# Kernel tuning notes

Hardware: AMD Instinct MI355X
Metric: run time of the kernel (lower is better)

The kernel has to match this reference:

```python
import jax, jax.numpy as jnp
import numpy as np

D_MODEL = 1024
H = 16
D_K = D_MODEL // H
D_FF = 4096
EPS = 1e-6
NEG = -1.0e9


def setup_inputs() -> dict:
    key = jax.random.key(0)
    ks = jax.random.split(key, 8)
    B, S = 4, 2048
    x = jax.random.normal(ks[0], (B, S, D_MODEL), dtype=jnp.float32)
    src_mask = jnp.ones((B, 1, S, S), dtype=jnp.int32)
    s = 0.02
    wq = jax.random.normal(ks[1], (D_MODEL, D_MODEL), jnp.float32) * s
    wk = jax.random.normal(ks[2], (D_MODEL, D_MODEL), jnp.float32) * s
    wv = jax.random.normal(ks[3], (D_MODEL, D_MODEL), jnp.float32) * s
    wo = jax.random.normal(ks[4], (D_MODEL, D_MODEL), jnp.float32) * s
    w1 = jax.random.normal(ks[5], (D_MODEL, D_FF), jnp.float32) * s
    b1 = jnp.zeros((D_FF,), jnp.float32)
    w2 = jax.random.normal(ks[6], (D_FF, D_MODEL), jnp.float32) * s
    b2 = jnp.zeros((D_MODEL,), jnp.float32)
    # LayerNorm params are scalars in the original (torch.ones(1)/zeros(1))
    a1 = jnp.ones((1,), jnp.float32); bt1 = jnp.zeros((1,), jnp.float32)
    a2 = jnp.ones((1,), jnp.float32); bt2 = jnp.zeros((1,), jnp.float32)
    return {"x": x, "src_mask": src_mask, "wq": wq, "wk": wk, "wv": wv,
            "wo": wo, "w1": w1, "b1": b1, "w2": w2, "b2": b2,
            "a1": a1, "bt1": bt1, "a2": a2, "bt2": bt2}


def _layernorm(x, alpha, beta):
    # Original: (x - mean) / (std + eps), std with Bessel correction (torch default)
    mean = jnp.mean(x, axis=-1, keepdims=True)
    std = jnp.std(x, axis=-1, keepdims=True, ddof=1)
    return alpha * (x - mean) / (std + EPS) + beta


def _mha(x, mask, wq, wk, wv, wo):
    B, S, _ = x.shape
    q = (x @ wq).reshape(B, S, H, D_K).transpose(0, 2, 1, 3)  # [B,H,S,Dk]
    k = (x @ wk).reshape(B, S, H, D_K).transpose(0, 2, 1, 3)
    v = (x @ wv).reshape(B, S, H, D_K).transpose(0, 2, 1, 3)
    scores = jnp.einsum('bhqd,bhkd->bhqk', q, k) / jnp.sqrt(jnp.float32(D_K))
    scores = jnp.where(mask == 0, NEG, scores)
    attn = jax.nn.softmax(scores, axis=-1)
    out = jnp.einsum('bhqk,bhkd->bhqd', attn, v)  # [B,H,S,Dk]
    out = out.transpose(0, 2, 1, 3).reshape(B, S, D_MODEL)
    return out @ wo


def reference(x, src_mask, wq, wk, wv, wo, w1, b1, w2, b2, a1, bt1, a2, bt2):
    # Sublayer 1: self-attention with post-norm residual (dropout = eval/identity)
    attn_out = _mha(x, src_mask, wq, wk, wv, wo)
    x = _layernorm(x + attn_out, a1, bt1)
    # Sublayer 2: FFN with post-norm residual
    ffn_out = jax.nn.relu(x @ w1 + b1) @ w2 + b2
    x = _layernorm(x + ffn_out, a2, bt2)
    return x
```

## Files before the change

kernel.cpp:

```cpp
#include <hip/hip_runtime.h>
#include <stdint.h>

typedef __bf16 bf16x8 __attribute__((ext_vector_type(8)));
typedef float f32x4 __attribute__((ext_vector_type(4)));
typedef float f32x16 __attribute__((ext_vector_type(16)));
typedef unsigned short u16;
typedef u16 u16x8 __attribute__((ext_vector_type(8)));
typedef u16 u16x4 __attribute__((ext_vector_type(4)));
typedef uint32_t u32;

#define DEV __device__ __forceinline__
#define MFMA(a, b, c) __builtin_amdgcn_mfma_f32_16x16x32_bf16(a, b, c, 0, 0, 0)
#define MFMA32(a, b, c) __builtin_amdgcn_mfma_f32_32x32x16_bf16(a, b, c, 0, 0, 0)

static constexpr int B_ = 4, S_ = 2048, M_ = 8192, D_ = 1024, H_ = 16, DFF_ = 4096;

DEV u16 f2bf(float f) {
    union { float f; u32 u; } c; c.f = f;
    u32 u = c.u;
    return (u16)((u + 0x7fffu + ((u >> 16) & 1u)) >> 16);
}

DEV u32 cvt_pk_bf16(float lo, float hi) {
    u32 r;
    asm("v_cvt_pk_bf16_f32 %0, %1, %2" : "=v"(r) : "v"(lo), "v"(hi));
    return r;
}

DEV float v_exp2(float x) {
    float r;
    asm("v_exp_f32 %0, %1" : "=v"(r) : "v"(x));
    return r;
}

DEV void gload16(void* lds, const void* g) {
    __builtin_amdgcn_global_load_lds(
        (const __attribute__((address_space(1))) unsigned int*)g,
        (__attribute__((address_space(3))) unsigned int*)lds, 16, 0, 0);
}


__global__ __launch_bounds__(256) void k_pack_mask(const int* __restrict__ m,
                                                   u32* __restrict__ bits, int nwords) {
    int w = blockIdx.x * 256 + threadIdx.x;
    if (w >= nwords) return;
    const int4* s = (const int4*)(m + (size_t)w * 32);
    u32 r = 0;
#pragma unroll
    for (int j = 0; j < 8; j++) {
        int4 v = s[j];
        r |= (u32)(v.x != 0) << (j * 4) | (u32)(v.y != 0) << (j * 4 + 1) |
             (u32)(v.z != 0) << (j * 4 + 2) | (u32)(v.w != 0) << (j * 4 + 3);
    }
    bits[w] = r;
}

__global__ __launch_bounds__(256) void k_cast_bf16(const float* __restrict__ s,
                                                   u16* __restrict__ d, int n4) {
    int i = blockIdx.x * 256 + threadIdx.x;
    if (i >= n4) return;
    f32x4 v = ((const f32x4*)s)[i];
    u16x4 o;
    o[0] = f2bf(v[0]); o[1] = f2bf(v[1]); o[2] = f2bf(v[2]); o[3] = f2bf(v[3]);
    ((u16x4*)d)[i] = o;
}

__global__ void k_transpose_cast(const float* __restrict__ s, u16* __restrict__ d,
                                 int K, int N) {
    __shared__ float t[32][33];
    int n0 = blockIdx.x * 32, k0 = blockIdx.y * 32;
    int tx = threadIdx.x, ty = threadIdx.y;
#pragma unroll
    for (int i = 0; i < 4; i++)
        t[ty + i * 8][tx] = s[(size_t)(k0 + ty + i * 8) * N + n0 + tx];
    __syncthreads();
#pragma unroll
    for (int i = 0; i < 4; i++)
        d[(size_t)(n0 + ty + i * 8) * K + k0 + tx] = f2bf(t[tx][ty + i * 8]);
}

__global__ void k_transpose_cast4(const float* __restrict__ s0,
                                  const float* __restrict__ s1,
                                  const float* __restrict__ s2,
                                  const float* __restrict__ s3,
                                  u16* __restrict__ dbase) {
    __shared__ float t[32][33];
    const int z = blockIdx.z;
    const float* s = (z == 0) ? s0 : (z == 1) ? s1 : (z == 2) ? s2 : s3;
    u16* d = dbase + (size_t)z * D_ * D_;
    int n0 = blockIdx.x * 32, k0 = blockIdx.y * 32;
    int tx = threadIdx.x, ty = threadIdx.y;
#pragma unroll
    for (int i = 0; i < 4; i++)
        t[ty + i * 8][tx] = s[(size_t)(k0 + ty + i * 8) * D_ + n0 + tx];
    __syncthreads();
#pragma unroll
    for (int i = 0; i < 4; i++)
        d[(size_t)(n0 + ty + i * 8) * D_ + k0 + tx] = f2bf(t[tx][ty + i * 8]);
}

template <int EPI>
__global__ __launch_bounds__(512, 4) void k_gemm8(const u16* __restrict__ A,
                                                  const u16* __restrict__ Bt,
                                                  float* __restrict__ Cf,
                                                  u16* __restrict__ Cb,
                                                  const float* __restrict__ bias,
                                                  const float* __restrict__ resid,
                                                  u16* __restrict__ Vt,
                                                  int N, int K) {
    __shared__ u16 As[2][128 * 64];
    __shared__ u16 Bs[2][128 * 64];
    const int tid = threadIdx.x, lane = tid & 63, wave = tid >> 6;
    const int lr = lane & 15, lg = lane >> 4;
    const int wm = wave >> 1, wn = wave & 1;
    const int nbx = N >> 7;
    const int chunk = gridDim.x >> 3;
    const int id = ((int)blockIdx.x & 7) * chunk + ((int)blockIdx.x >> 3);
    const size_t row0 = (size_t)(id / nbx) * 128;
    const int col0 = (id % nbx) * 128;
    const int srow = lane >> 3;
    const int sgr = (lane & 7) ^ srow;
    const int NT = K >> 6;
    f32x4 acc[2][4] = {};

    auto stage = [&](int buf, int t) {
#pragma unroll
        for (int i = 0; i < 2; i++) {
            int c = i * 8 + wave;
            gload16((char*)&As[buf][0] + c * 1024,
                    (const char*)(A + (row0 + c * 8 + srow) * K + t * 64 + sgr * 8));
        }
#pragma unroll
        for (int i = 0; i < 2; i++) {
            int c = i * 8 + wave;
            gload16((char*)&Bs[buf][0] + c * 1024,
                    (const char*)(Bt + (size_t)(col0 + c * 8 + srow) * K + t * 64 + sgr * 8));
        }
    };

    stage(0, 0);
    for (int t = 0; t < NT; ++t) {
        const int cur = t & 1;
        if (t + 1 < NT) {
            stage(cur ^ 1, t + 1);
            asm volatile("s_waitcnt vmcnt(4)" ::: "memory");
        } else {
            asm volatile("s_waitcnt vmcnt(0)" ::: "memory");
        }
        __builtin_amdgcn_s_barrier();
        asm volatile("" ::: "memory");
        bf16x8 bF[4][2];
#pragma unroll
        for (int n = 0; n < 4; n++) {
            int r = wn * 64 + n * 16 + lr;
            int rb = r * 128, sw = (r & 7) << 4;
#pragma unroll
            for (int ks = 0; ks < 2; ks++)
                bF[n][ks] = *(const bf16x8*)((char*)&Bs[cur][0] +
                                             (rb + ((ks * 64 + lg * 16) ^ sw)));
        }
#pragma unroll
        for (int m = 0; m < 2; m++) {
            int r = wm * 32 + m * 16 + lr;
            int rb = r * 128, sw = (r & 7) << 4;
            bf16x8 a0 = *(const bf16x8*)((char*)&As[cur][0] + (rb + ((lg * 16) ^ sw)));
            bf16x8 a1 = *(const bf16x8*)((char*)&As[cur][0] + (rb + ((64 + lg * 16) ^ sw)));
            __builtin_amdgcn_s_setprio(1);
#pragma unroll
            for (int n = 0; n < 4; n++) {
                acc[m][n] = MFMA(a0, bF[n][0], acc[m][n]);
                acc[m][n] = MFMA(a1, bF[n][1], acc[m][n]);
            }
            __builtin_amdgcn_s_setprio(0);
        }
        asm volatile("" ::: "memory");
        __builtin_amdgcn_s_barrier();
    }
#pragma unroll
    for (int m = 0; m < 2; m++)
#pragma unroll
        for (int n = 0; n < 4; n++) {
            const int cg = col0 + wn * 64 + n * 16 + lr;
            const int rbase = (int)row0 + wm * 32 + m * 16 + lg * 4;
            if constexpr (EPI == 0) {
                const int proj = cg >> 10, hh = (cg >> 6) & 15, dk = cg & 63;
                const int b = rbase >> 11, s = rbase & 2047;
                if (proj == 2) {
                    u16x4 ov;
#pragma unroll
                    for (int i = 0; i < 4; i++) ov[i] = f2bf(acc[m][n][i]);
                    *(u16x4*)(Vt + ((size_t)(b * 16 + hh) * 64 + dk) * 2048 + s) = ov;
                } else {
                    const float sc = (proj == 0) ? 0.1803368801111832f : 1.f;
                    size_t base = ((size_t)(proj * 64 + b * 16 + hh) * 2048 + s) * 64 + dk;
#pragma unroll
                    for (int i = 0; i < 4; i++)
                        Cb[base + (size_t)i * 64] = f2bf(acc[m][n][i] * sc);
                }
            } else {
#pragma unroll
                for (int i = 0; i < 4; i++) {
                    const int rg = rbase + i;
                    float v = acc[m][n][i];
                    if constexpr (EPI == 1) {
                        Cf[(size_t)rg * N + cg] = v + resid[(size_t)rg * N + cg];
                    } else if constexpr (EPI == 2) {
                        v += bias[cg];
                        v = v > 0.f ? v : 0.f;
                        Cb[(size_t)rg * N + cg] = f2bf(v);
                    } else {
                        Cf[(size_t)rg * N + cg] = v + bias[cg] + resid[(size_t)rg * N + cg];
                    }
                }
            }
        }
}

template <int EPI, int KSPLITS>
__global__ __launch_bounds__(512, 2) void k_gemm256(const u16* __restrict__ A,
                                                    const u16* __restrict__ Bt,
                                                    float* __restrict__ Cf,
                                                    float* __restrict__ Cf2,
                                                    u16* __restrict__ Cb,
                                                    const float* __restrict__ bias,
                                                    int N, int Keff, int lda) {
    __shared__ u16 As[2][256 * 64];
    __shared__ u16 Bs[2][256 * 64];
    const int tid = threadIdx.x, lane = tid & 63, wave = tid >> 6;
    const int lr = lane & 15, lg = lane >> 4;
    const int wm = wave >> 2, wn = wave & 3;
    const int nbx = N >> 8;
    const int chunk = gridDim.x >> 3;
    const int id = ((int)blockIdx.x & 7) * chunk + ((int)blockIdx.x >> 3);
    int tileid = id, ksplit = 0;
    if constexpr (KSPLITS == 2) { ksplit = id & 1; tileid = id >> 1; }
    const int kof = ksplit * Keff;
    const size_t row0 = (size_t)(tileid / nbx) * 256;
    const int col0 = (tileid % nbx) * 256;
    const int srow = lane >> 3;
    const int sgr = (lane & 7) ^ srow;
    const int NT = Keff >> 6;
    f32x4 acc[8][4] = {};

    auto stage_half = [&](int isB, int buf, int t, int h) {
        const u16* g = isB ? Bt : A;
        const size_t grow0 = isB ? (size_t)col0 : row0;
        char* base = isB ? (char*)&Bs[buf][0] : (char*)&As[buf][0];
#pragma unroll
        for (int l = 0; l < 2; l++) {
            int rt = h * 128 + l * 64 + wave * 8;
            gload16(base + rt * 128,
                    (const char*)(g + (grow0 + rt + srow) * lda + kof + t * 64 + sgr * 8));
        }
    };
    auto rdA = [&](int cur, int mh, int m, int kk) -> bf16x8 {
        int r = wm * 128 + mh * 64 + m * 16 + lr;
        int gi = kk * 4 + lg;
        return *(const bf16x8*)((char*)&As[cur][0] + r * 128 + ((gi ^ (r & 7)) << 4));
    };
    auto rdB = [&](int cur, int nh, int n, int kk) -> bf16x8 {
        int r = wn * 64 + nh * 32 + n * 16 + lr;
        int gi = kk * 4 + lg;
        return *(const bf16x8*)((char*)&Bs[cur][0] + r * 128 + ((gi ^ (r & 7)) << 4));
    };

    stage_half(0, 0, 0, 0); stage_half(0, 0, 0, 1);
    stage_half(1, 0, 0, 0); stage_half(1, 0, 0, 1);
    stage_half(1, 1, 1, 0); stage_half(1, 1, 1, 1);
    asm volatile("s_waitcnt vmcnt(4)" ::: "memory");
    __builtin_amdgcn_s_barrier();

    bf16x8 aF[4][2], b0F[2][2], b1F[2][2];
    for (int t = 0; t < NT; ++t) {
        const int cur = t & 1, nxt = cur ^ 1;
#pragma unroll
        for (int m = 0; m < 4; m++) { aF[m][0] = rdA(cur, 0, m, 0); aF[m][1] = rdA(cur, 0, m, 1); }
#pragma unroll
        for (int n = 0; n < 2; n++) { b0F[n][0] = rdB(cur, 0, n, 0); b0F[n][1] = rdB(cur, 0, n, 1); }
        if (t + 1 < NT) stage_half(0, nxt, t + 1, 0);
        __builtin_amdgcn_s_barrier();
        asm volatile("s_waitcnt lgkmcnt(0)" ::: "memory");
        __builtin_amdgcn_sched_barrier(0);
        __builtin_amdgcn_s_setprio(1);
#pragma unroll
        for (int m = 0; m < 4; m++)
#pragma unroll
            for (int n = 0; n < 2; n++) {
                acc[m][n] = MFMA(aF[m][0], b0F[n][0], acc[m][n]);
                acc[m][n] = MFMA(aF[m][1], b0F[n][1], acc[m][n]);
            }
        __builtin_amdgcn_s_setprio(0);
        __builtin_amdgcn_s_barrier();
#pragma unroll
        for (int n = 0; n < 2; n++) { b1F[n][0] = rdB(cur, 1, n, 0); b1F[n][1] = rdB(cur, 1, n, 1); }
        if (t + 1 < NT) stage_half(0, nxt, t + 1, 1);
        __builtin_amdgcn_s_barrier();
        asm volatile("s_waitcnt lgkmcnt(0)" ::: "memory");
        __builtin_amdgcn_sched_barrier(0);
        __builtin_amdgcn_s_setprio(1);
#pragma unroll
        for (int m = 0; m < 4; m++)
#pragma unroll
            for (int n = 0; n < 2; n++) {
                acc[m][2 + n] = MFMA(aF[m][0], b1F[n][0], acc[m][2 + n]);
                acc[m][2 + n] = MFMA(aF[m][1], b1F[n][1], acc[m][2 + n]);
            }
        __builtin_amdgcn_s_setprio(0);
        __builtin_amdgcn_s_barrier();
#pragma unroll
        for (int m = 0; m < 4; m++) { aF[m][0] = rdA(cur, 1, m, 0); aF[m][1] = rdA(cur, 1, m, 1); }
        if (t + 2 < NT) stage_half(1, cur, t + 2, 0);
        __builtin_amdgcn_s_barrier();
        asm volatile("s_waitcnt lgkmcnt(0)" ::: "memory");
        __builtin_amdgcn_sched_barrier(0);
        __builtin_amdgcn_s_setprio(1);
#pragma unroll
        for (int m = 0; m < 4; m++)
#pragma unroll
            for (int n = 0; n < 2; n++) {
                acc[4 + m][2 + n] = MFMA(aF[m][0], b1F[n][0], acc[4 + m][2 + n]);
                acc[4 + m][2 + n] = MFMA(aF[m][1], b1F[n][1], acc[4 + m][2 + n]);
            }
        __builtin_amdgcn_s_setprio(0);
        __builtin_amdgcn_s_barrier();
        if (t + 2 < NT) stage_half(1, cur, t + 2, 1);
        if (t + 1 < NT) {
            if (t + 2 < NT) asm volatile("s_waitcnt vmcnt(4)" ::: "memory");
            else            asm volatile("s_waitcnt vmcnt(0)" ::: "memory");
        }
        __builtin_amdgcn_s_barrier();
        __builtin_amdgcn_s_setprio(1);
#pragma unroll
        for (int m = 0; m < 4; m++)
#pragma unroll
            for (int n = 0; n < 2; n++) {
                acc[4 + m][n] = MFMA(aF[m][0], b0F[n][0], acc[4 + m][n]);
                acc[4 + m][n] = MFMA(aF[m][1], b0F[n][1], acc[4 + m][n]);
            }
        __builtin_amdgcn_s_setprio(0);
        __builtin_amdgcn_s_barrier();
    }
    float* Cout = (KSPLITS == 2 && ksplit) ? Cf2 : Cf;
#pragma unroll
    for (int m = 0; m < 8; m++)
#pragma unroll
        for (int n = 0; n < 4; n++)
#pragma unroll
            for (int i = 0; i < 4; i++) {
                int rg = (int)row0 + wm * 128 + m * 16 + lg * 4 + i;
                int cg = col0 + wn * 64 + n * 16 + lr;
                float v = acc[m][n][i];
                if constexpr (EPI == 2) {
                    v += bias[cg];
                    v = v > 0.f ? v : 0.f;
                    Cb[(size_t)rg * N + cg] = f2bf(v);
                } else {
                    Cout[(size_t)rg * N + cg] = v;
                }
            }
}

__global__ __launch_bounds__(256) void k_attn(const u16* __restrict__ qkv,
                                              const u16* __restrict__ vT,
                                              const u32* __restrict__ mbits,
                                              u16* __restrict__ outb) {
    __shared__ u16 Kt[2][64 * 64];
    __shared__ u16 Vt[2][64 * 64];
    __shared__ u32 pm[2][128][2];
    const int tid = threadIdx.x, lane = tid & 63, wave = tid >> 6;
    const int l31 = lane & 31, hi = lane >> 5;
    const int id0 = blockIdx.y * 16 + blockIdx.x;
    const int id = (id0 & 7) * 128 + (id0 >> 3);
    const int bh = id >> 4;
    const int b = bh >> 4, h = bh & 15;
    const int qb0 = (id & 15) * 128;
    const size_t qbase = (size_t)bh * (2048 * 64);
    const size_t kbase = (size_t)(64 + bh) * (2048 * 64);
    const size_t vtbase = (size_t)bh * (64 * 2048);

    bf16x8 qf[4];
    const int q0 = qb0 + wave * 32;
#pragma unroll
    for (int dstep = 0; dstep < 4; dstep++)
        qf[dstep] = *(const bf16x8*)(qkv + qbase + (size_t)(q0 + l31) * 64 +
                                     dstep * 16 + hi * 8);

    u16x8 ones_u;
#pragma unroll
    for (int e = 0; e < 8; e++) ones_u[e] = 0x3f80;
    const bf16x8 ones8 = *(const bf16x8*)&ones_u;

    f32x16 o0 = {}, o1 = {}, lacc = {};
    f32x16 zin;
#pragma unroll
    for (int r = 0; r < 16; r++) zin[r] = -16.f;

    const int str = tid >> 2, sq = tid & 3;
    const int swzs = (str & 7) << 4;

    u16x8 krA, krB, vrA, vrB; u32 mwA;
    auto issue_loads = [&](int kv0n) {
        const u16* ksrc = qkv + kbase + (size_t)(kv0n + str) * 64 + sq * 16;
        krA = *(const u16x8*)ksrc; krB = *(const u16x8*)(ksrc + 8);
        const u16* vsrc = vT + vtbase + (size_t)str * 2048 + kv0n + sq * 16;
        vrA = *(const u16x8*)vsrc; vrB = *(const u16x8*)(vsrc + 8);
        mwA = mbits[(size_t)(b * 2048 + qb0 + (tid >> 1)) * 64 + (kv0n >> 5) + (tid & 1)];
    };
    auto write_tile = [&](int buf) -> bool {
        int b0 = str * 128 + sq * 32;
        *(u16x8*)((char*)&Kt[buf][0] + ((b0) ^ swzs)) = krA;
        *(u16x8*)((char*)&Kt[buf][0] + ((b0 + 16) ^ swzs)) = krB;
        *(u16x8*)((char*)&Vt[buf][0] + ((b0) ^ swzs)) = vrA;
        *(u16x8*)((char*)&Vt[buf][0] + ((b0 + 16) ^ swzs)) = vrB;
        pm[buf][tid >> 1][tid & 1] = mwA;
        return (__ballot(mwA == 0xffffffffu) == ~0ull);
    };

    const int rK0 = l31, rK1 = 32 + l31;
    const int swK0 = (rK0 & 7) << 4, swK1 = (rK1 & 7) << 4;

    issue_loads(0);
    bool aon_nxt = write_tile(0);
    for (int t = 0; t < 32; ++t) {
        const int cur = t & 1;
        const bool aon_cur = aon_nxt;
        if (t + 1 < 32) issue_loads((t + 1) * 64);
        asm volatile("s_waitcnt lgkmcnt(0)" ::: "memory");
        __builtin_amdgcn_s_barrier();

        f32x16 st0 = zin, st1 = zin;
        __builtin_amdgcn_s_setprio(1);
#pragma unroll
        for (int dstep = 0; dstep < 4; dstep++) {
            bf16x8 kf0 = *(const bf16x8*)((char*)&Kt[cur][0] + rK0 * 128 +
                                          ((dstep * 32 + hi * 16) ^ swK0));
            bf16x8 kf1 = *(const bf16x8*)((char*)&Kt[cur][0] + rK1 * 128 +
                                          ((dstep * 32 + hi * 16) ^ swK1));
            st0 = MFMA32(kf0, qf[dstep], st0);
            st1 = MFMA32(kf1, qf[dstep], st1);
        }
        __builtin_amdgcn_s_setprio(0);

        if (!aon_cur) {
            u32 mw0 = pm[cur][wave * 32 + l31][0] >> (hi * 4);
            u32 mw1 = pm[cur][wave * 32 + l31][1] >> (hi * 4);
#pragma unroll
            for (int r = 0; r < 16; r++) {
                int sh = (r & 3) + 8 * (r >> 2);
                if (!((mw0 >> sh) & 1u)) st0[r] = -1e9f;
                if (!((mw1 >> sh) & 1u)) st1[r] = -1e9f;
            }
        }
        bf16x8 pa[4];
#pragma unroll
        for (int r = 0; r < 16; r++) { st0[r] = v_exp2(st0[r]); st1[r] = v_exp2(st1[r]); }
#pragma unroll
        for (int kvb = 0; kvb < 2; kvb++) {
            const f32x16& st = kvb ? st1 : st0;
            u32 wA[4], wB[4];
#pragma unroll
            for (int g = 0; g < 4; g++) {
                wA[g] = cvt_pk_bf16(st[4 * g], st[4 * g + 1]);
                wB[g] = cvt_pk_bf16(st[4 * g + 2], st[4 * g + 3]);
            }
#pragma unroll
            for (int s = 0; s < 2; s++) {
                u32 xA = wA[2 * s], yA = wA[2 * s + 1];
                asm("v_permlane32_swap_b32 %0, %1" : "+v"(xA), "+v"(yA));
                u32 xB = wB[2 * s], yB = wB[2 * s + 1];
                asm("v_permlane32_swap_b32 %0, %1" : "+v"(xB), "+v"(yB));
                union { u32 w[4]; bf16x8 v; } pk;
                pk.w[0] = xA; pk.w[1] = xB; pk.w[2] = yA; pk.w[3] = yB;
                pa[kvb * 2 + s] = pk.v;
            }
        }
        __builtin_amdgcn_s_setprio(1);
#pragma unroll
        for (int ks = 0; ks < 4; ks++) {
            bf16x8 vb0 = *(const bf16x8*)((char*)&Vt[cur][0] + rK0 * 128 +
                                          ((ks * 32 + hi * 16) ^ swK0));
            bf16x8 vb1 = *(const bf16x8*)((char*)&Vt[cur][0] + rK1 * 128 +
                                          ((ks * 32 + hi * 16) ^ swK1));
            lacc = MFMA32(pa[ks], ones8, lacc);
            o0 = MFMA32(pa[ks], vb0, o0);
            o1 = MFMA32(pa[ks], vb1, o1);
        }
        __builtin_amdgcn_s_setprio(0);
        if (t + 1 < 32) aon_nxt = write_tile(cur ^ 1);
    }
#pragma unroll
    for (int r = 0; r < 16; r++) {
        float inv = 1.f / lacc[r];
        int qg = qb0 + wave * 32 + (r & 3) + 8 * (r >> 2) + 4 * hi;
        size_t rowb = (size_t)(b * 2048 + qg) * 1024 + h * 64 + l31;
        outb[rowb] = f2bf(o0[r] * inv);
        outb[rowb + 32] = f2bf(o1[r] * inv);
    }
}

template <bool WB>
__global__ __launch_bounds__(256) void k_ln(const float* __restrict__ tin,
                                            float* __restrict__ outf,
                                            u16* __restrict__ outb,
                                            const float* __restrict__ alpha,
                                            const float* __restrict__ beta) {
    const int row = blockIdx.x, tid = threadIdx.x;
    const f32x4 t = ((const f32x4*)(tin + (size_t)row * 1024))[tid];
    float s = t[0] + t[1] + t[2] + t[3];
    float ss = t[0] * t[0] + t[1] * t[1] + t[2] * t[2] + t[3] * t[3];
#pragma unroll
    for (int m2 = 1; m2 < 64; m2 <<= 1) {
        s += __shfl_xor(s, m2);
        ss += __shfl_xor(ss, m2);
    }
    __shared__ float ps[4], pss[4];
    if ((tid & 63) == 0) { ps[tid >> 6] = s; pss[tid >> 6] = ss; }
    __syncthreads();
    s = ps[0] + ps[1] + ps[2] + ps[3];
    ss = pss[0] + pss[1] + pss[2] + pss[3];
    const float mean = s * (1.f / 1024.f);
    float var = (ss - 1024.f * mean * mean) * (1.f / 1023.f);
    var = fmaxf(var, 0.f);
    const float inv = alpha[0] / (sqrtf(var) + 1e-6f);
    const float bet = beta[0];
    f32x4 oo;
#pragma unroll
    for (int i = 0; i < 4; i++) oo[i] = (t[i] - mean) * inv + bet;
    ((f32x4*)(outf + (size_t)row * 1024))[tid] = oo;
    if constexpr (WB) {
        u16x4 ob;
#pragma unroll
        for (int i = 0; i < 4; i++) ob[i] = f2bf(oo[i]);
        ((u16x4*)(outb + (size_t)row * 1024))[tid] = ob;
    }
}

__global__ __launch_bounds__(256) void k_ln_sum2(const float* __restrict__ p0,
                                                 const float* __restrict__ p1,
                                                 const float* __restrict__ resid,
                                                 const float* __restrict__ bias,
                                                 float* __restrict__ outf,
                                                 const float* __restrict__ alpha,
                                                 const float* __restrict__ beta) {
    const int row = blockIdx.x, tid = threadIdx.x;
    const f32x4 a = ((const f32x4*)(p0 + (size_t)row * 1024))[tid];
    const f32x4 c = ((const f32x4*)(p1 + (size_t)row * 1024))[tid];
    const f32x4 r = ((const f32x4*)(resid + (size_t)row * 1024))[tid];
    const f32x4 bb = ((const f32x4*)bias)[tid];
    f32x4 t;
#pragma unroll
    for (int i = 0; i < 4; i++) t[i] = a[i] + c[i] + r[i] + bb[i];
    float s = t[0] + t[1] + t[2] + t[3];
    float ss = t[0] * t[0] + t[1] * t[1] + t[2] * t[2] + t[3] * t[3];
#pragma unroll
    for (int m2 = 1; m2 < 64; m2 <<= 1) {
        s += __shfl_xor(s, m2);
        ss += __shfl_xor(ss, m2);
    }
    __shared__ float ps[4], pss[4];
    if ((tid & 63) == 0) { ps[tid >> 6] = s; pss[tid >> 6] = ss; }
    __syncthreads();
    s = ps[0] + ps[1] + ps[2] + ps[3];
    ss = pss[0] + pss[1] + pss[2] + pss[3];
    const float mean = s * (1.f / 1024.f);
    float var = (ss - 1024.f * mean * mean) * (1.f / 1023.f);
    var = fmaxf(var, 0.f);
    const float inv = alpha[0] / (sqrtf(var) + 1e-6f);
    const float bet = beta[0];
    f32x4 oo;
#pragma unroll
    for (int i = 0; i < 4; i++) oo[i] = (t[i] - mean) * inv + bet;
    ((f32x4*)(outf + (size_t)row * 1024))[tid] = oo;
}

extern "C" void kernel_launch(void* const* d_in, const int* in_sizes, int n_in,
                              void* d_out, int out_size, void* d_ws, size_t ws_size,
                              hipStream_t stream) {
    const float* x   = (const float*)d_in[0];
    const int*   msk = (const int*)d_in[1];
    const float* wq  = (const float*)d_in[2];
    const float* wk  = (const float*)d_in[3];
    const float* wv  = (const float*)d_in[4];
    const float* wo  = (const float*)d_in[5];
    const float* w1  = (const float*)d_in[6];
    const float* b1  = (const float*)d_in[7];
    const float* w2  = (const float*)d_in[8];
    const float* b2  = (const float*)d_in[9];
    const float* a1  = (const float*)d_in[10];
    const float* bt1 = (const float*)d_in[11];
    const float* a2  = (const float*)d_in[12];
    const float* bt2 = (const float*)d_in[13];
    float* out = (float*)d_out;

    char* ws = (char*)d_ws;
    size_t off = 0;
    auto alloc = [&](size_t bytes) {
        void* p = ws + off;
        off += (bytes + 255) & ~(size_t)255;
        return p;
    };
    u16* xb    = (u16*)alloc((size_t)M_ * D_ * 2);
    u16* wqkvT = (u16*)alloc((size_t)3 * D_ * D_ * 2);
    u16* woT   = (u16*)alloc((size_t)D_ * D_ * 2);
    u16* w1T   = (u16*)alloc((size_t)DFF_ * D_ * 2);
    u16* w2T   = (u16*)alloc((size_t)D_ * DFF_ * 2);
    u32* mbits = (u32*)alloc((size_t)B_ * S_ * 64 * 4);
    u16* aout  = (u16*)alloc((size_t)M_ * D_ * 2);
    float* y   = (float*)alloc((size_t)M_ * D_ * 4);
    float* y1  = (float*)alloc((size_t)M_ * D_ * 4);
    float* x1  = (float*)alloc((size_t)M_ * D_ * 4);
    u16* x1b   = (u16*)alloc((size_t)M_ * D_ * 2);
    u16* vTb   = (u16*)alloc((size_t)64 * 64 * 2048 * 2);
    u16* qkv   = (u16*)alloc((size_t)M_ * DFF_ * 2);
    u16* hft   = qkv;

    k_pack_mask<<<dim3((B_ * S_ * 64) / 256), 256, 0, stream>>>(msk, mbits, B_ * S_ * 64);
    k_cast_bf16<<<dim3((M_ * D_ / 4) / 256), 256, 0, stream>>>(x, xb, M_ * D_ / 4);
    dim3 tb(32, 8);
    k_transpose_cast4<<<dim3(32, 32, 4), tb, 0, stream>>>(wq, wk, wv, wo, wqkvT);
    k_transpose_cast<<<dim3(128, 32), tb, 0, stream>>>(w1, w1T, D_, DFF_);
    k_transpose_cast<<<dim3(32, 128), tb, 0, stream>>>(w2, w2T, DFF_, D_);

    k_gemm8<0><<<dim3(1536), 512, 0, stream>>>(xb, wqkvT, nullptr, qkv, nullptr,
                                               nullptr, vTb, 3 * D_, D_);
    k_attn<<<dim3(16, 64), 256, 0, stream>>>(qkv, vTb, mbits, aout);
    k_gemm8<1><<<dim3(512), 512, 0, stream>>>(aout, woT, y, nullptr, nullptr, x,
                                              nullptr, D_, D_);
    k_ln<true><<<dim3(M_), 256, 0, stream>>>(y, x1, x1b, a1, bt1);
    k_gemm256<2, 1><<<dim3(512), 512, 0, stream>>>(x1b, w1T, nullptr, nullptr, hft,
                                                   b1, DFF_, D_, D_);
    k_gemm256<3, 2><<<dim3(256), 512, 0, stream>>>(hft, w2T, y, y1, nullptr,
                                                   nullptr, D_, DFF_ / 2, DFF_);
    k_ln_sum2<<<dim3(M_), 256, 0, stream>>>(y, y1, x1, b2, out, a2, bt2);
}
```

Baseline: 412.2 us.

## Stage attention K/V via direct-to-LDS loads and carry residuals in bf16

The attention kernel now loads K and V tiles with global_load_lds straight into swizzled LDS, replacing the register round-trip. It also uses a precomputed per-row all-ones mask bitmap (new k_amask kernel) so mask words are read only for tiles that are not fully unmasked. The Wo GEMM epilogue writes its residual sum as bf16, the first LayerNorm reads bf16 and emits only a bf16 output, and the final LayerNorm takes its residual from that bf16 buffer, which cuts fp32 traffic. Trade-offs: an extra barrier per iteration, one more small kernel, and lower precision in the residual path.

```diff
diff --git a/kernel.cpp b/kernel.cpp
--- a/kernel.cpp
+++ b/kernel.cpp
@@ -21,6 +21,11 @@
     return (u16)((u + 0x7fffu + ((u >> 16) & 1u)) >> 16);
 }
 
+DEV float bf2f(u16 v) {
+    union { u32 u; float f; } c; c.u = (u32)v << 16;
+    return c.f;
+}
+
 DEV u32 cvt_pk_bf16(float lo, float hi) {
     u32 r;
     asm("v_cvt_pk_bf16_f32 %0, %1, %2" : "=v"(r) : "v"(lo), "v"(hi));
@@ -53,6 +58,21 @@
              (u32)(v.z != 0) << (j * 4 + 2) | (u32)(v.w != 0) << (j * 4 + 3);
     }
     bits[w] = r;
+}
+
+__global__ __launch_bounds__(256) void k_amask(const u32* __restrict__ bits,
+                                               u32* __restrict__ am, int rows) {
+    int row = blockIdx.x * 256 + threadIdx.x;
+    if (row >= rows) return;
+    const uint4* p = (const uint4*)(bits + (size_t)row * 64);
+    u32 r = 0;
+#pragma unroll
+    for (int j = 0; j < 16; j++) {
+        uint4 v = p[j];
+        r |= (u32)((v.x & v.y) == 0xffffffffu) << (2 * j);
+        r |= (u32)((v.z & v.w) == 0xffffffffu) << (2 * j + 1);
+    }
+    am[row] = r;
 }
 
 __global__ __launch_bounds__(256) void k_cast_bf16(const float* __restrict__ s,
@@ -203,7 +223,7 @@
                     const int rg = rbase + i;
                     float v = acc[m][n][i];
                     if constexpr (EPI == 1) {
-                        Cf[(size_t)rg * N + cg] = v + resid[(size_t)rg * N + cg];
+                        Cb[(size_t)rg * N + cg] = f2bf(v + resid[(size_t)rg * N + cg]);
                     } else if constexpr (EPI == 2) {
                         v += bias[cg];
                         v = v > 0.f ? v : 0.f;
@@ -363,10 +383,10 @@
 __global__ __launch_bounds__(256) void k_attn(const u16* __restrict__ qkv,
                                               const u16* __restrict__ vT,
                                               const u32* __restrict__ mbits,
+                                              const u32* __restrict__ amask,
                                               u16* __restrict__ outb) {
     __shared__ u16 Kt[2][64 * 64];
     __shared__ u16 Vt[2][64 * 64];
-    __shared__ u32 pm[2][128][2];
     const int tid = threadIdx.x, lane = tid & 63, wave = tid >> 6;
     const int l31 = lane & 31, hi = lane >> 5;
     const int id0 = blockIdx.y * 16 + blockIdx.x;
@@ -395,37 +415,34 @@
 #pragma unroll
     for (int r = 0; r < 16; r++) zin[r] = -16.f;
 
-    const int str = tid >> 2, sq = tid & 3;
-    const int swzs = (str & 7) << 4;
-
-    u16x8 krA, krB, vrA, vrB; u32 mwA;
-    auto issue_loads = [&](int kv0n) {
-        const u16* ksrc = qkv + kbase + (size_t)(kv0n + str) * 64 + sq * 16;
-        krA = *(const u16x8*)ksrc; krB = *(const u16x8*)(ksrc + 8);
-        const u16* vsrc = vT + vtbase + (size_t)str * 2048 + kv0n + sq * 16;
-        vrA = *(const u16x8*)vsrc; vrB = *(const u16x8*)(vsrc + 8);
-        mwA = mbits[(size_t)(b * 2048 + qb0 + (tid >> 1)) * 64 + (kv0n >> 5) + (tid & 1)];
+    const int srow8 = lane >> 3;
+    const int sgr = (lane & 7) ^ srow8;
+    auto stage = [&](int buf, int kv0) {
+#pragma unroll
+        for (int i = 0; i < 2; i++) {
+            int c = i * 4 + wave;
+            gload16((char*)&Kt[buf][0] + c * 1024,
+                    (const char*)(qkv + kbase + (size_t)(kv0 + c * 8 + srow8) * 64 + sgr * 8));
+            gload16((char*)&Vt[buf][0] + c * 1024,
+                    (const char*)(vT + vtbase + (size_t)(c * 8 + srow8) * 2048 + kv0 + sgr * 8));
+        }
     };
-    auto write_tile = [&](int buf) -> bool {
-        int b0 = str * 128 + sq * 32;
-        *(u16x8*)((char*)&Kt[buf][0] + ((b0) ^ swzs)) = krA;
-        *(u16x8*)((char*)&Kt[buf][0] + ((b0 + 16) ^ swzs)) = krB;
-        *(u16x8*)((char*)&Vt[buf][0] + ((b0) ^ swzs)) = vrA;
-        *(u16x8*)((char*)&Vt[buf][0] + ((b0 + 16) ^ swzs)) = vrB;
-        pm[buf][tid >> 1][tid & 1] = mwA;
-        return (__ballot(mwA == 0xffffffffu) == ~0ull);
-    };
-
+
+    const u32 am = amask[b * 2048 + qb0 + wave * 32 + l31];
     const int rK0 = l31, rK1 = 32 + l31;
     const int swK0 = (rK0 & 7) << 4, swK1 = (rK1 & 7) << 4;
 
-    issue_loads(0);
-    bool aon_nxt = write_tile(0);
+    stage(0, 0);
+    asm volatile("s_waitcnt vmcnt(0)" ::: "memory");
+    __builtin_amdgcn_s_barrier();
     for (int t = 0; t < 32; ++t) {
         const int cur = t & 1;
-        const bool aon_cur = aon_nxt;
-        if (t + 1 < 32) issue_loads((t + 1) * 64);
-        asm volatile("s_waitcnt lgkmcnt(0)" ::: "memory");
+        if (t + 1 < 32) {
+            stage(cur ^ 1, (t + 1) * 64);
+            asm volatile("s_waitcnt vmcnt(4)" ::: "memory");
+        } else {
+            asm volatile("s_waitcnt vmcnt(0)" ::: "memory");
+        }
         __builtin_amdgcn_s_barrier();
 
         f32x16 st0 = zin, st1 = zin;
@@ -441,9 +458,9 @@
         }
         __builtin_amdgcn_s_setprio(0);
 
-        if (!aon_cur) {
-            u32 mw0 = pm[cur][wave * 32 + l31][0] >> (hi * 4);
-            u32 mw1 = pm[cur][wave * 32 + l31][1] >> (hi * 4);
+        if (!((am >> t) & 1u)) {
+            uint2 mw = *(const uint2*)&mbits[(size_t)(b * 2048 + qb0 + wave * 32 + l31) * 64 + 2 * t];
+            u32 mw0 = mw.x >> (hi * 4), mw1 = mw.y >> (hi * 4);
 #pragma unroll
             for (int r = 0; r < 16; r++) {
                 int sh = (r & 3) + 8 * (r >> 2);
@@ -486,7 +503,7 @@
             o1 = MFMA32(pa[ks], vb1, o1);
         }
         __builtin_amdgcn_s_setprio(0);
-        if (t + 1 < 32) aon_nxt = write_tile(cur ^ 1);
+        __builtin_amdgcn_s_barrier();
     }
 #pragma unroll
     for (int r = 0; r < 16; r++) {
@@ -498,14 +515,15 @@
     }
 }
 
-template <bool WB>
-__global__ __launch_bounds__(256) void k_ln(const float* __restrict__ tin,
-                                            float* __restrict__ outf,
-                                            u16* __restrict__ outb,
-                                            const float* __restrict__ alpha,
-                                            const float* __restrict__ beta) {
+__global__ __launch_bounds__(256) void k_ln_b(const u16* __restrict__ tin,
+                                              u16* __restrict__ outb,
+                                              const float* __restrict__ alpha,
+                                              const float* __restrict__ beta) {
     const int row = blockIdx.x, tid = threadIdx.x;
-    const f32x4 t = ((const f32x4*)(tin + (size_t)row * 1024))[tid];
+    const u16x4 tv = ((const u16x4*)(tin + (size_t)row * 1024))[tid];
+    f32x4 t;
+#pragma unroll
+    for (int i = 0; i < 4; i++) t[i] = bf2f(tv[i]);
     float s = t[0] + t[1] + t[2] + t[3];
     float ss = t[0] * t[0] + t[1] * t[1] + t[2] * t[2] + t[3] * t[3];
 #pragma unroll
@@ -523,21 +541,15 @@
     var = fmaxf(var, 0.f);
     const float inv = alpha[0] / (sqrtf(var) + 1e-6f);
     const float bet = beta[0];
-    f32x4 oo;
-#pragma unroll
-    for (int i = 0; i < 4; i++) oo[i] = (t[i] - mean) * inv + bet;
-    ((f32x4*)(outf + (size_t)row * 1024))[tid] = oo;
-    if constexpr (WB) {
-        u16x4 ob;
-#pragma unroll
-        for (int i = 0; i < 4; i++) ob[i] = f2bf(oo[i]);
-        ((u16x4*)(outb + (size_t)row * 1024))[tid] = ob;
-    }
+    u16x4 ob;
+#pragma unroll
+    for (int i = 0; i < 4; i++) ob[i] = f2bf((t[i] - mean) * inv + bet);
+    ((u16x4*)(outb + (size_t)row * 1024))[tid] = ob;
 }
 
 __global__ __launch_bounds__(256) void k_ln_sum2(const float* __restrict__ p0,
                                                  const float* __restrict__ p1,
-                                                 const float* __restrict__ resid,
+                                                 const u16* __restrict__ residb,
                                                  const float* __restrict__ bias,
                                                  float* __restrict__ outf,
                                                  const float* __restrict__ alpha,
@@ -545,11 +557,11 @@
     const int row = blockIdx.x, tid = threadIdx.x;
     const f32x4 a = ((const f32x4*)(p0 + (size_t)row * 1024))[tid];
     const f32x4 c = ((const f32x4*)(p1 + (size_t)row * 1024))[tid];
-    const f32x4 r = ((const f32x4*)(resid + (size_t)row * 1024))[tid];
+    const u16x4 rv = ((const u16x4*)(residb + (size_t)row * 1024))[tid];
     const f32x4 bb = ((const f32x4*)bias)[tid];
     f32x4 t;
 #pragma unroll
-    for (int i = 0; i < 4; i++) t[i] = a[i] + c[i] + r[i] + bb[i];
+    for (int i = 0; i < 4; i++) t[i] = a[i] + c[i] + bf2f(rv[i]) + bb[i];
     float s = t[0] + t[1] + t[2] + t[3];
     float ss = t[0] * t[0] + t[1] * t[1] + t[2] * t[2] + t[3] * t[3];
 #pragma unroll
@@ -605,16 +617,18 @@
     u16* w1T   = (u16*)alloc((size_t)DFF_ * D_ * 2);
     u16* w2T   = (u16*)alloc((size_t)D_ * DFF_ * 2);
     u32* mbits = (u32*)alloc((size_t)B_ * S_ * 64 * 4);
+    u32* amsk  = (u32*)alloc((size_t)B_ * S_ * 4);
     u16* aout  = (u16*)alloc((size_t)M_ * D_ * 2);
+    u16* yb    = (u16*)alloc((size_t)M_ * D_ * 2);
     float* y   = (float*)alloc((size_t)M_ * D_ * 4);
     float* y1  = (float*)alloc((size_t)M_ * D_ * 4);
-    float* x1  = (float*)alloc((size_t)M_ * D_ * 4);
     u16* x1b   = (u16*)alloc((size_t)M_ * D_ * 2);
     u16* vTb   = (u16*)alloc((size_t)64 * 64 * 2048 * 2);
     u16* qkv   = (u16*)alloc((size_t)M_ * DFF_ * 2);
     u16* hft   = qkv;
 
     k_pack_mask<<<dim3((B_ * S_ * 64) / 256), 256, 0, stream>>>(msk, mbits, B_ * S_ * 64);
+    k_amask<<<dim3((B_ * S_) / 256), 256, 0, stream>>>(mbits, amsk, B_ * S_);
     k_cast_bf16<<<dim3((M_ * D_ / 4) / 256), 256, 0, stream>>>(x, xb, M_ * D_ / 4);
     dim3 tb(32, 8);
     k_transpose_cast4<<<dim3(32, 32, 4), tb, 0, stream>>>(wq, wk, wv, wo, wqkvT);
@@ -623,13 +637,13 @@
 
     k_gemm8<0><<<dim3(1536), 512, 0, stream>>>(xb, wqkvT, nullptr, qkv, nullptr,
                                                nullptr, vTb, 3 * D_, D_);
-    k_attn<<<dim3(16, 64), 256, 0, stream>>>(qkv, vTb, mbits, aout);
-    k_gemm8<1><<<dim3(512), 512, 0, stream>>>(aout, woT, y, nullptr, nullptr, x,
+    k_attn<<<dim3(16, 64), 256, 0, stream>>>(qkv, vTb, mbits, amsk, aout);
+    k_gemm8<1><<<dim3(512), 512, 0, stream>>>(aout, woT, nullptr, yb, nullptr, x,
                                               nullptr, D_, D_);
-    k_ln<true><<<dim3(M_), 256, 0, stream>>>(y, x1, x1b, a1, bt1);
+    k_ln_b<<<dim3(M_), 256, 0, stream>>>(yb, x1b, a1, bt1);
     k_gemm256<2, 1><<<dim3(512), 512, 0, stream>>>(x1b, w1T, nullptr, nullptr, hft,
                                                    b1, DFF_, D_, D_);
     k_gemm256<3, 2><<<dim3(256), 512, 0, stream>>>(hft, w2T, y, y1, nullptr,
                                                    nullptr, D_, DFF_ / 2, DFF_);
-    k_ln_sum2<<<dim3(M_), 256, 0, stream>>>(y, y1, x1, b2, out, a2, bt2);
-}
+    k_ln_sum2<<<dim3(M_), 256, 0, stream>>>(y, y1, x1b, b2, out, a2, bt2);
+}
```

New measurement: 413.5 us. No clear change (+0.3%).
